# Performance work log

Measured on AMD Instinct MI355X. Metric: run time of the kernel, lower is better.

## Reference

```python
import jax, jax.numpy as jnp
import numpy as np

EPS = 1e-5

def setup_inputs() -> dict:
    key = jax.random.key(0)
    ks = jax.random.split(key, 8)
    N, C, ST, LT = 32, 2048, 16, 400
    ALPHA, K, BETA, CK = 4, 3, 4, 3
    Cb = C // BETA
    inp = {
        'st_feat': jax.random.normal(ks[0], (N, C, ST, 1, 1), dtype=jnp.float32),
        'lt_feat': jax.random.normal(ks[1], (N, C, LT, 1, 1), dtype=jnp.float32),
        # global branch G: Linear(ST->ST*alpha) -> BN1d -> ReLU -> Linear(->K) -> softmax
        'g_w1': jax.random.normal(ks[2], (ST * ALPHA, ST), dtype=jnp.float32) * 0.02,
        'g_bn_gamma': jnp.ones((ST * ALPHA,), jnp.float32),
        'g_bn_beta': jnp.zeros((ST * ALPHA,), jnp.float32),
        'g_bn_mean': jnp.zeros((ST * ALPHA,), jnp.float32),
        'g_bn_var': jnp.ones((ST * ALPHA,), jnp.float32),
        'g_w2': jax.random.normal(ks[3], (K, ST * ALPHA), dtype=jnp.float32) * 0.02,
        # local branch L: Conv1d(C->C/beta,k=3) -> BN1d -> ReLU -> Conv1d(C/beta->C,1) -> sigmoid
        'l_w1': jax.random.normal(ks[4], (Cb, C, CK), dtype=jnp.float32) * 0.02,
        'l_bn_gamma': jnp.ones((Cb,), jnp.float32),
        'l_bn_beta': jnp.zeros((Cb,), jnp.float32),
        'l_bn_mean': jnp.zeros((Cb,), jnp.float32),
        'l_bn_var': jnp.ones((Cb,), jnp.float32),
        'l_w2': jax.random.normal(ks[5], (C, Cb), dtype=jnp.float32) * 0.02,
    }
    return inp


def reference(st_feat, lt_feat, g_w1, g_bn_gamma, g_bn_beta, g_bn_mean, g_bn_var,
              g_w2, l_w1, l_bn_gamma, l_bn_beta, l_bn_mean, l_bn_var, l_w2):
    N, C, ST = st_feat.shape[:3]
    LT = lt_feat.shape[2]
    K = g_w2.shape[0]
    PAD = 1  # adaptive_convolution_padding; stride = 1
    # ---- global branch: per-(n,c) adaptive kernel (h=w=1 so avgpool is identity)
    st = st_feat.reshape(N * C, ST)                               # [NC, ST]
    h = st @ g_w1.T                                               # [NC, ST*alpha]
    h = (h - g_bn_mean) * jax.lax.rsqrt(g_bn_var + EPS) * g_bn_gamma + g_bn_beta
    h = jax.nn.relu(h)
    conv_kernel = jax.nn.softmax(h @ g_w2.T, axis=-1)             # [NC, K]
    # ---- local branch: channel-temporal sigmoid gate
    lt = lt_feat.reshape(N, C, LT)                                # [N, C, LT]
    x = jax.lax.conv_general_dilated(lt, l_w1, window_strides=(1,),
                                     padding=[(1, 1)],
                                     dimension_numbers=('NCH', 'OIH', 'NCH'))  # [N, C/beta, LT]
    x = (x - l_bn_mean[None, :, None]) * jax.lax.rsqrt(l_bn_var + EPS)[None, :, None] \
        * l_bn_gamma[None, :, None] + l_bn_beta[None, :, None]
    x = jax.nn.relu(x)
    gate = jax.nn.sigmoid(jnp.einsum('oc,nct->not', l_w2, x))     # [N, C, LT]
    new_lt = lt * gate
    # ---- temporal adaptive aggregation: per-(n,c) depthwise 1D conv, K taps
    kern = conv_kernel.reshape(N, C, K)
    xp = jnp.pad(new_lt, ((0, 0), (0, 0), (PAD, PAD)))            # [N, C, LT+2*PAD]
    out_len = LT + 2 * PAD - K + 1                                # == LT for K=3, PAD=1
    out = jnp.zeros((N, C, out_len), dtype=new_lt.dtype)
    for i in range(K):  # K is tiny (3)
        out = out + kern[:, :, i:i + 1] * xp[:, :, i:i + out_len]
    return out.reshape(N, C, out_len, 1, 1)
```

## Files before the change

kernel.cpp:

```cpp
#include <hip/hip_runtime.h>
#include <hip/hip_bf16.h>

#define N_   32
#define C_   2048
#define ST_  16
#define H_   64
#define K_   3
#define CB_  512
#define LT_  400
#define LTP_ 402
#define BK   32
#define TSTR 126

using bf16x8 = __attribute__((ext_vector_type(8))) __bf16;
using f32x4  = __attribute__((ext_vector_type(4))) float;
typedef unsigned short ushort_t;

__device__ __forceinline__ unsigned short f2bf(float f) {
    unsigned int u = __float_as_uint(f);
    u = (u + 0x7fffu + ((u >> 16) & 1u)) >> 16;
    return (unsigned short)u;
}
__device__ __forceinline__ float bf2f(unsigned short h) {
    return __uint_as_float(((unsigned int)h) << 16);
}
__device__ __forceinline__ void gload16(const ushort_t* g, ushort_t* l) {
    __builtin_amdgcn_global_load_lds(
        (const __attribute__((address_space(1))) unsigned int*)g,
        (__attribute__((address_space(3))) unsigned int*)l, 16, 0, 0);
}

__global__ __launch_bounds__(256) void k_global(
    const float* __restrict__ st, const float* __restrict__ g_w1,
    const float* __restrict__ gam, const float* __restrict__ bet,
    const float* __restrict__ mean, const float* __restrict__ var,
    const float* __restrict__ g_w2, float* __restrict__ kern) {
    __shared__ float w1[H_][ST_];
    __shared__ float sc[H_], bi[H_];
    __shared__ float w2[K_][H_];
    int tid = threadIdx.x;
    for (int i = tid; i < H_ * ST_; i += 256) w1[i / ST_][i % ST_] = g_w1[i];
    if (tid < H_) {
        float s = gam[tid] * rsqrtf(var[tid] + 1e-5f);
        sc[tid] = s;
        bi[tid] = bet[tid] - mean[tid] * s;
    }
    for (int i = tid; i < K_ * H_; i += 256) w2[i / H_][i % H_] = g_w2[i];
    __syncthreads();
    int row = blockIdx.x * 256 + tid;
    const float* p = st + (size_t)row * ST_;
    float s[ST_];
#pragma unroll
    for (int i = 0; i < ST_; ++i) s[i] = p[i];
    float lg0 = 0.f, lg1 = 0.f, lg2 = 0.f;
    for (int j = 0; j < H_; ++j) {
        float h = 0.f;
#pragma unroll
        for (int i = 0; i < ST_; ++i) h = fmaf(w1[j][i], s[i], h);
        h = fmaxf(fmaf(h, sc[j], bi[j]), 0.f);
        lg0 = fmaf(w2[0][j], h, lg0);
        lg1 = fmaf(w2[1][j], h, lg1);
        lg2 = fmaf(w2[2][j], h, lg2);
    }
    float m = fmaxf(lg0, fmaxf(lg1, lg2));
    float e0 = __expf(lg0 - m), e1 = __expf(lg1 - m), e2 = __expf(lg2 - m);
    float inv = 1.f / (e0 + e1 + e2);
    float4 o = make_float4(e0 * inv, e1 * inv, e2 * inv, 0.f);
    *(float4*)(kern + (size_t)row * 4) = o;
}

__global__ __launch_bounds__(256) void k_transpose(
    const float* __restrict__ lt, ushort_t* __restrict__ ltT) {
    __shared__ float tile[32][33];
    int tt0 = blockIdx.x * 32;
    int cc  = blockIdx.y * 32;
    int n   = blockIdx.z;
    const float* src = lt + ((size_t)n * C_ + cc) * LT_;
    int tx = threadIdx.x & 31, ty = threadIdx.x >> 5;
#pragma unroll
    for (int i = 0; i < 4; ++i) {
        int c = ty + i * 8;
        int t = tt0 + tx;
        tile[c][tx] = (t < LT_) ? src[(size_t)c * LT_ + t] : 0.f;
    }
    __syncthreads();
    int cx  = (threadIdx.x & 15) * 2;
    int tyw = threadIdx.x >> 4;
    unsigned int* dst = (unsigned int*)(ltT + (size_t)n * LTP_ * C_ + cc + cx);
#pragma unroll
    for (int i = 0; i < 2; ++i) {
        int tl = tyw + i * 16;
        int t = tt0 + tl;
        if (t < LT_) {
            unsigned int v = (unsigned int)f2bf(tile[cx][tl]) |
                             ((unsigned int)f2bf(tile[cx + 1][tl]) << 16);
            dst[(size_t)(t + 1) * (C_ / 2)] = v;
        }
    }
}

__global__ __launch_bounds__(256) void k_zero(ushort_t* __restrict__ ltT) {
    int i = blockIdx.x * 256 + threadIdx.x;
    int n = i >> 11, c = i & (C_ - 1);
    size_t base = (size_t)n * LTP_ * C_;
    ltT[base + c] = 0;
    ltT[base + (size_t)(LTP_ - 1) * C_ + c] = 0;
}

__global__ __launch_bounds__(256) void k_w1(
    const float* __restrict__ l_w1, ushort_t* __restrict__ w1b) {
    int i = blockIdx.x * 256 + threadIdx.x;
    float a = l_w1[(size_t)i * 3 + 0];
    float b = l_w1[(size_t)i * 3 + 1];
    float c = l_w1[(size_t)i * 3 + 2];
    w1b[0 * (size_t)CB_ * C_ + i] = f2bf(a);
    w1b[1 * (size_t)CB_ * C_ + i] = f2bf(b);
    w1b[2 * (size_t)CB_ * C_ + i] = f2bf(c);
}

__global__ __launch_bounds__(256) void k_w2(
    const float* __restrict__ l_w2, ushort_t* __restrict__ w2b) {
    int i = blockIdx.x * 256 + threadIdx.x;
    w2b[i] = f2bf(l_w2[i]);
}

__global__ __launch_bounds__(256, 2) void k_gemm1(
    const ushort_t* __restrict__ ltT, const ushort_t* __restrict__ w1b,
    const float* __restrict__ bn_g, const float* __restrict__ bn_b,
    const float* __restrict__ bn_m, const float* __restrict__ bn_v,
    ushort_t* __restrict__ Xws) {
    __shared__ __align__(16) ushort_t Asm[2 * 128 * BK];
    __shared__ __align__(16) ushort_t Bsm[2 * 384 * BK];
    const int tid = threadIdx.x;
    const int n   = blockIdx.z;
    const int tm  = blockIdx.x * TSTR;
    const int cb0 = blockIdx.y * 128;
    const int lane = tid & 63, lrow = lane & 15, quad = lane >> 4;
    const int wv = tid >> 6, wvM = wv & 1, wvN = wv >> 1;

    const int srow = lane >> 2;
    const int csrc = (((lane & 3) ^ ((lane >> 3) & 3)) << 3);
    const ushort_t* gA[2];
#pragma unroll
    for (int i = 0; i < 2; ++i) {
        int r = (2 * wv + i) * 16 + srow;
        int gr = tm + r; gr = gr < LTP_ - 1 ? gr : LTP_ - 1;
        gA[i] = ltT + ((size_t)n * LTP_ + gr) * C_ + csrc;
    }
    const ushort_t* gB[6];
#pragma unroll
    for (int j = 0; j < 6; ++j) {
        int r = (6 * wv + j) * 16 + srow;
        gB[j] = w1b + ((size_t)((r >> 7) * CB_ + cb0 + (r & 127))) * C_ + csrc;
    }
    const int sB = lrow * BK + ((quad ^ ((lrow >> 1) & 3)) << 3);
    int sA[3];
#pragma unroll
    for (int k = 0; k < 3; ++k)
        sA[k] = (lrow + k) * BK + ((quad ^ (((lrow + k) >> 1) & 3)) << 3);

    f32x4 acc[4][4];
#pragma unroll
    for (int i = 0; i < 4; ++i)
#pragma unroll
        for (int j = 0; j < 4; ++j) acc[i][j] = (f32x4){0.f, 0.f, 0.f, 0.f};

#define STAGE1(buf)                                                         \
    {                                                                       \
        ushort_t* ad = Asm + (buf) * (128 * BK) + (2 * wv) * (16 * BK);     \
        gload16(gA[0], ad);                                                 \
        gload16(gA[1], ad + 16 * BK);                                       \
        gA[0] += BK; gA[1] += BK;                                           \
        ushort_t* bd = Bsm + (buf) * (384 * BK) + (6 * wv) * (16 * BK);     \
        _Pragma("unroll")                                                   \
        for (int j = 0; j < 6; ++j) {                                       \
            gload16(gB[j], bd + j * (16 * BK));                             \
            gB[j] += BK;                                                    \
        }                                                                   \
    }

    STAGE1(0);
    for (int s = 0; s < C_ / BK; ++s) {
        __syncthreads();
        const int cur = s & 1;
        if (s + 1 < C_ / BK) STAGE1(cur ^ 1);
        const ushort_t* Ab = Asm + cur * (128 * BK) + wvM * (64 * BK);
        const ushort_t* Bb = Bsm + cur * (384 * BK) + wvN * (64 * BK) + sB;
        bf16x8 bfr[3][4];
#pragma unroll
        for (int k = 0; k < 3; ++k)
#pragma unroll
            for (int nf = 0; nf < 4; ++nf)
                bfr[k][nf] = *(const bf16x8*)(Bb + k * (128 * BK) + nf * (16 * BK));
#pragma unroll
        for (int mf = 0; mf < 4; ++mf) {
            bf16x8 af[3];
#pragma unroll
            for (int k = 0; k < 3; ++k)
                af[k] = *(const bf16x8*)(Ab + sA[k] + mf * (16 * BK));
#pragma unroll
            for (int nf = 0; nf < 4; ++nf)
#pragma unroll
                for (int k = 0; k < 3; ++k)
                    acc[mf][nf] = __builtin_amdgcn_mfma_f32_16x16x32_bf16(af[k], bfr[k][nf], acc[mf][nf], 0, 0, 0);
        }
    }
#undef STAGE1
    float sc[4], bo[4];
#pragma unroll
    for (int nf = 0; nf < 4; ++nf) {
        int cb = cb0 + wvN * 64 + nf * 16 + lrow;
        float s0 = bn_g[cb] * rsqrtf(bn_v[cb] + 1e-5f);
        sc[nf] = s0;
        bo[nf] = bn_b[cb] - bn_m[cb] * s0;
    }
#pragma unroll
    for (int mf = 0; mf < 4; ++mf) {
#pragma unroll
        for (int r = 0; r < 4; ++r) {
            int local = wvM * 64 + mf * 16 + quad * 4 + r;
            int t = tm + local;
            if (local < TSTR && t < LT_) {
#pragma unroll
                for (int nf = 0; nf < 4; ++nf) {
                    int cb = cb0 + wvN * 64 + nf * 16 + lrow;
                    float v = fmaxf(fmaf(acc[mf][nf][r], sc[nf], bo[nf]), 0.f);
                    Xws[((size_t)n * LT_ + t) * CB_ + cb] = f2bf(v);
                }
            }
        }
    }
}

__global__ __launch_bounds__(256, 3) void k_gemm2(
    const ushort_t* __restrict__ Xws, const ushort_t* __restrict__ w2b,
    ushort_t* __restrict__ gate) {
    __shared__ __align__(16) ushort_t Asm[2 * 128 * BK];
    __shared__ __align__(16) ushort_t Bsm[2 * 128 * BK];
    const int tid = threadIdx.x;
    const int n  = blockIdx.z;
    const int cm = blockIdx.x * 128;
    const int tt = blockIdx.y * 128;
    const int lane = tid & 63, lrow = lane & 15, quad = lane >> 4;
    const int wv = tid >> 6, wvM = wv & 1, wvN = wv >> 1;

    const int srow = lane >> 2;
    const int csrc = (((lane & 3) ^ ((lane >> 3) & 3)) << 3);
    const ushort_t* gA[2];
    const ushort_t* gB[2];
#pragma unroll
    for (int i = 0; i < 2; ++i) {
        int r = (2 * wv + i) * 16 + srow;
        gA[i] = w2b + (size_t)(cm + r) * CB_ + csrc;
        int tr = tt + r; tr = tr < LT_ - 1 ? tr : LT_ - 1;
        gB[i] = Xws + ((size_t)n * LT_ + tr) * CB_ + csrc;
    }
    const int sOff = lrow * BK + ((quad ^ ((lrow >> 1) & 3)) << 3);

    f32x4 acc[4][4];
#pragma unroll
    for (int i = 0; i < 4; ++i)
#pragma unroll
        for (int j = 0; j < 4; ++j) acc[i][j] = (f32x4){0.f, 0.f, 0.f, 0.f};

#define STAGE2(buf)                                                         \
    {                                                                       \
        ushort_t* ad = Asm + (buf) * (128 * BK) + (2 * wv) * (16 * BK);     \
        ushort_t* bd = Bsm + (buf) * (128 * BK) + (2 * wv) * (16 * BK);     \
        gload16(gA[0], ad);                                                 \
        gload16(gA[1], ad + 16 * BK);                                       \
        gload16(gB[0], bd);                                                 \
        gload16(gB[1], bd + 16 * BK);                                       \
        gA[0] += BK; gA[1] += BK; gB[0] += BK; gB[1] += BK;                 \
    }

    STAGE2(0);
    for (int s = 0; s < CB_ / BK; ++s) {
        __syncthreads();
        const int cur = s & 1;
        if (s + 1 < CB_ / BK) STAGE2(cur ^ 1);
        const ushort_t* Ab = Asm + cur * (128 * BK) + wvM * (64 * BK) + sOff;
        const ushort_t* Bb = Bsm + cur * (128 * BK) + wvN * (64 * BK) + sOff;
        bf16x8 af[4], bfm[4];
#pragma unroll
        for (int mf = 0; mf < 4; ++mf)
            af[mf] = *(const bf16x8*)(Ab + mf * (16 * BK));
#pragma unroll
        for (int nf = 0; nf < 4; ++nf)
            bfm[nf] = *(const bf16x8*)(Bb + nf * (16 * BK));
#pragma unroll
        for (int mf = 0; mf < 4; ++mf)
#pragma unroll
            for (int nf = 0; nf < 4; ++nf)
                acc[mf][nf] = __builtin_amdgcn_mfma_f32_16x16x32_bf16(af[mf], bfm[nf], acc[mf][nf], 0, 0, 0);
    }
#undef STAGE2
#pragma unroll
    for (int mf = 0; mf < 4; ++mf) {
#pragma unroll
        for (int r = 0; r < 4; ++r) {
            int c = cm + wvM * 64 + mf * 16 + quad * 4 + r;
#pragma unroll
            for (int nf = 0; nf < 4; ++nf) {
                int t = tt + wvN * 64 + nf * 16 + lrow;
                if (t < LT_) {
                    float g = 1.f / (1.f + __expf(-acc[mf][nf][r]));
                    gate[((size_t)n * C_ + c) * LT_ + t] = f2bf(g);
                }
            }
        }
    }
}

__global__ __launch_bounds__(256) void k_final(
    const float* __restrict__ lt, const ushort_t* __restrict__ gate,
    const float* __restrict__ kern, float* __restrict__ out) {
    long long idx = (long long)blockIdx.x * 256 + threadIdx.x;
    int t0 = (int)(idx % 100) * 4;
    long long nc = idx / 100;
    const float*   ltp = lt   + (size_t)nc * LT_;
    const ushort_t* gp = gate + (size_t)nc * LT_;
    float4 kv = *(const float4*)(kern + (size_t)nc * 4);
    float nl[6];
#pragma unroll
    for (int j = -1; j <= 4; ++j) {
        int t = t0 + j;
        nl[j + 1] = (t >= 0 && t < LT_) ? ltp[t] * bf2f(gp[t]) : 0.f;
    }
    float4 o;
    o.x = kv.x * nl[0] + kv.y * nl[1] + kv.z * nl[2];
    o.y = kv.x * nl[1] + kv.y * nl[2] + kv.z * nl[3];
    o.z = kv.x * nl[2] + kv.y * nl[3] + kv.z * nl[4];
    o.w = kv.x * nl[3] + kv.y * nl[4] + kv.z * nl[5];
    *(float4*)(out + (size_t)nc * LT_ + t0) = o;
}

extern "C" void kernel_launch(void* const* d_in, const int* in_sizes, int n_in,
                              void* d_out, int out_size, void* d_ws, size_t ws_size,
                              hipStream_t stream) {
    const float* st   = (const float*)d_in[0];
    const float* lt   = (const float*)d_in[1];
    const float* g_w1 = (const float*)d_in[2];
    const float* g_bg = (const float*)d_in[3];
    const float* g_bb = (const float*)d_in[4];
    const float* g_bm = (const float*)d_in[5];
    const float* g_bv = (const float*)d_in[6];
    const float* g_w2 = (const float*)d_in[7];
    const float* l_w1 = (const float*)d_in[8];
    const float* l_bg = (const float*)d_in[9];
    const float* l_bb = (const float*)d_in[10];
    const float* l_bm = (const float*)d_in[11];
    const float* l_bv = (const float*)d_in[12];
    const float* l_w2 = (const float*)d_in[13];
    float* out = (float*)d_out;

    char* ws = (char*)d_ws;
    float*    kern = (float*)(ws + 0);
    ushort_t* w1b  = (ushort_t*)(ws + 1048576);
    ushort_t* w2b  = (ushort_t*)(ws + 7340032);
    ushort_t* Xws  = (ushort_t*)(ws + 9437184);
    ushort_t* ltT  = (ushort_t*)(ws + 22544384);
    ushort_t* gate = ltT;

    k_global<<<dim3((N_ * C_) / 256), dim3(256), 0, stream>>>(
        st, g_w1, g_bg, g_bb, g_bm, g_bv, g_w2, kern);
    k_w1<<<dim3((CB_ * C_) / 256), dim3(256), 0, stream>>>(l_w1, w1b);
    k_w2<<<dim3((C_ * CB_) / 256), dim3(256), 0, stream>>>(l_w2, w2b);
    k_zero<<<dim3((N_ * C_) / 256), dim3(256), 0, stream>>>(ltT);
    k_transpose<<<dim3(13, C_ / 32, N_), dim3(256), 0, stream>>>(lt, ltT);
    k_gemm1<<<dim3(4, 4, N_), dim3(256), 0, stream>>>(
        ltT, w1b, l_bg, l_bb, l_bm, l_bv, Xws);
    k_gemm2<<<dim3(C_ / 128, 4, N_), dim3(256), 0, stream>>>(Xws, w2b, gate);
    k_final<<<dim3((N_ * C_ * (LT_ / 4)) / 256), dim3(256), 0, stream>>>(
        lt, gate, kern, out);
}
```

Measured before the change: 425.1 us.

## Triple-buffer GEMM pipelines, enlarge gemm1 tiles, flatten gemm2 over N*LT, widen final

Both GEMMs switch from double to triple-buffered LDS staging, using explicit vmcnt waits, raw barriers and setprio around the MFMA blocks so loads stay further in flight. gemm1 moves to 512-thread blocks covering 254 time rows each, so every batch needs two tiles instead of four and the large weight B tile is loaded half as often. gemm2 flattens batch and time into one dimension (12800 = 100*128), which removes the partial time tile and its wasted work. The final kernel processes 8 outputs per thread with vectorised loads. The extra LDS and 512-thread blocks may reduce occupancy.

```diff
diff --git a/kernel.cpp b/kernel.cpp
--- a/kernel.cpp
+++ b/kernel.cpp
@@ -10,7 +10,7 @@
 #define LT_  400
 #define LTP_ 402
 #define BK   32
-#define TSTR 126
+#define TV1  254
 
 using bf16x8 = __attribute__((ext_vector_type(8))) __bf16;
 using f32x4  = __attribute__((ext_vector_type(4))) float;
@@ -124,19 +124,21 @@
     w2b[i] = f2bf(l_w2[i]);
 }
 
-__global__ __launch_bounds__(256, 2) void k_gemm1(
+__global__ __launch_bounds__(512, 2) void k_gemm1(
     const ushort_t* __restrict__ ltT, const ushort_t* __restrict__ w1b,
     const float* __restrict__ bn_g, const float* __restrict__ bn_b,
     const float* __restrict__ bn_m, const float* __restrict__ bn_v,
     ushort_t* __restrict__ Xws) {
-    __shared__ __align__(16) ushort_t Asm[2 * 128 * BK];
-    __shared__ __align__(16) ushort_t Bsm[2 * 384 * BK];
+    __shared__ __align__(16) ushort_t Asm[3 * 256 * BK + 2 * BK];
+    __shared__ __align__(16) ushort_t Bsm[3 * 384 * BK];
     const int tid = threadIdx.x;
-    const int n   = blockIdx.z;
-    const int tm  = blockIdx.x * TSTR;
+    const int mseg = blockIdx.x;
+    const int n   = mseg >> 1;
+    const int tm  = (mseg & 1) * TV1;
     const int cb0 = blockIdx.y * 128;
     const int lane = tid & 63, lrow = lane & 15, quad = lane >> 4;
-    const int wv = tid >> 6, wvM = wv & 1, wvN = wv >> 1;
+    const int wv = tid >> 6;
+    const int wvM = wv >> 1, wvN = wv & 1;
 
     const int srow = lane >> 2;
     const int csrc = (((lane & 3) ^ ((lane >> 3) & 3)) << 3);
@@ -147,11 +149,11 @@
         int gr = tm + r; gr = gr < LTP_ - 1 ? gr : LTP_ - 1;
         gA[i] = ltT + ((size_t)n * LTP_ + gr) * C_ + csrc;
     }
-    const ushort_t* gB[6];
-#pragma unroll
-    for (int j = 0; j < 6; ++j) {
-        int r = (6 * wv + j) * 16 + srow;
-        gB[j] = w1b + ((size_t)((r >> 7) * CB_ + cb0 + (r & 127))) * C_ + csrc;
+    const ushort_t* gB[3];
+#pragma unroll
+    for (int j = 0; j < 3; ++j) {
+        int rB = (3 * wv + j) * 16 + srow;
+        gB[j] = w1b + ((size_t)((rB >> 7) * CB_ + cb0 + (rB & 127))) * C_ + csrc;
     }
     const int sB = lrow * BK + ((quad ^ ((lrow >> 1) & 3)) << 3);
     int sA[3];
@@ -167,24 +169,31 @@
 
 #define STAGE1(buf)                                                         \
     {                                                                       \
-        ushort_t* ad = Asm + (buf) * (128 * BK) + (2 * wv) * (16 * BK);     \
+        ushort_t* ad = Asm + (buf) * (256 * BK) + (2 * wv) * (16 * BK);     \
         gload16(gA[0], ad);                                                 \
         gload16(gA[1], ad + 16 * BK);                                       \
         gA[0] += BK; gA[1] += BK;                                           \
-        ushort_t* bd = Bsm + (buf) * (384 * BK) + (6 * wv) * (16 * BK);     \
-        _Pragma("unroll")                                                   \
-        for (int j = 0; j < 6; ++j) {                                       \
-            gload16(gB[j], bd + j * (16 * BK));                             \
-            gB[j] += BK;                                                    \
-        }                                                                   \
+        ushort_t* bd = Bsm + (buf) * (384 * BK) + (3 * wv) * (16 * BK);     \
+        gload16(gB[0], bd);                                                 \
+        gload16(gB[1], bd + 16 * BK);                                       \
+        gload16(gB[2], bd + 32 * BK);                                       \
+        gB[0] += BK; gB[1] += BK; gB[2] += BK;                              \
     }
 
     STAGE1(0);
+    STAGE1(1);
+    int cur = 0, pre = 2;
     for (int s = 0; s < C_ / BK; ++s) {
-        __syncthreads();
-        const int cur = s & 1;
-        if (s + 1 < C_ / BK) STAGE1(cur ^ 1);
-        const ushort_t* Ab = Asm + cur * (128 * BK) + wvM * (64 * BK);
+        if (s < C_ / BK - 1) asm volatile("s_waitcnt vmcnt(5)" ::: "memory");
+        else                 asm volatile("s_waitcnt vmcnt(0)" ::: "memory");
+        __builtin_amdgcn_sched_barrier(0);
+        __builtin_amdgcn_s_barrier();
+        __builtin_amdgcn_sched_barrier(0);
+        if (s < C_ / BK - 2) {
+            STAGE1(pre);
+            pre = (pre == 2) ? 0 : pre + 1;
+        }
+        const ushort_t* Ab = Asm + cur * (256 * BK) + wvM * (64 * BK);
         const ushort_t* Bb = Bsm + cur * (384 * BK) + wvN * (64 * BK) + sB;
         bf16x8 bfr[3][4];
 #pragma unroll
@@ -192,6 +201,7 @@
 #pragma unroll
             for (int nf = 0; nf < 4; ++nf)
                 bfr[k][nf] = *(const bf16x8*)(Bb + k * (128 * BK) + nf * (16 * BK));
+        __builtin_amdgcn_s_setprio(1);
 #pragma unroll
         for (int mf = 0; mf < 4; ++mf) {
             bf16x8 af[3];
@@ -204,6 +214,8 @@
                 for (int k = 0; k < 3; ++k)
                     acc[mf][nf] = __builtin_amdgcn_mfma_f32_16x16x32_bf16(af[k], bfr[k][nf], acc[mf][nf], 0, 0, 0);
         }
+        __builtin_amdgcn_s_setprio(0);
+        cur = (cur == 2) ? 0 : cur + 1;
     }
 #undef STAGE1
     float sc[4], bo[4];
@@ -220,7 +232,7 @@
         for (int r = 0; r < 4; ++r) {
             int local = wvM * 64 + mf * 16 + quad * 4 + r;
             int t = tm + local;
-            if (local < TSTR && t < LT_) {
+            if (local < TV1 && t < LT_) {
 #pragma unroll
                 for (int nf = 0; nf < 4; ++nf) {
                     int cb = cb0 + wvN * 64 + nf * 16 + lrow;
@@ -235,12 +247,11 @@
 __global__ __launch_bounds__(256, 3) void k_gemm2(
     const ushort_t* __restrict__ Xws, const ushort_t* __restrict__ w2b,
     ushort_t* __restrict__ gate) {
-    __shared__ __align__(16) ushort_t Asm[2 * 128 * BK];
-    __shared__ __align__(16) ushort_t Bsm[2 * 128 * BK];
+    __shared__ __align__(16) ushort_t Asm[3 * 128 * BK];
+    __shared__ __align__(16) ushort_t Bsm[3 * 128 * BK];
     const int tid = threadIdx.x;
-    const int n  = blockIdx.z;
-    const int cm = blockIdx.x * 128;
-    const int tt = blockIdx.y * 128;
+    const int cm  = blockIdx.x * 128;
+    const int fn0 = blockIdx.y * 128;
     const int lane = tid & 63, lrow = lane & 15, quad = lane >> 4;
     const int wv = tid >> 6, wvM = wv & 1, wvN = wv >> 1;
 
@@ -252,8 +263,7 @@
     for (int i = 0; i < 2; ++i) {
         int r = (2 * wv + i) * 16 + srow;
         gA[i] = w2b + (size_t)(cm + r) * CB_ + csrc;
-        int tr = tt + r; tr = tr < LT_ - 1 ? tr : LT_ - 1;
-        gB[i] = Xws + ((size_t)n * LT_ + tr) * CB_ + csrc;
+        gB[i] = Xws + (size_t)(fn0 + r) * CB_ + csrc;
     }
     const int sOff = lrow * BK + ((quad ^ ((lrow >> 1) & 3)) << 3);
 
@@ -275,10 +285,18 @@
     }
 
     STAGE2(0);
+    STAGE2(1);
+    int cur = 0, pre = 2;
     for (int s = 0; s < CB_ / BK; ++s) {
-        __syncthreads();
-        const int cur = s & 1;
-        if (s + 1 < CB_ / BK) STAGE2(cur ^ 1);
+        if (s < CB_ / BK - 1) asm volatile("s_waitcnt vmcnt(4)" ::: "memory");
+        else                  asm volatile("s_waitcnt vmcnt(0)" ::: "memory");
+        __builtin_amdgcn_sched_barrier(0);
+        __builtin_amdgcn_s_barrier();
+        __builtin_amdgcn_sched_barrier(0);
+        if (s < CB_ / BK - 2) {
+            STAGE2(pre);
+            pre = (pre == 2) ? 0 : pre + 1;
+        }
         const ushort_t* Ab = Asm + cur * (128 * BK) + wvM * (64 * BK) + sOff;
         const ushort_t* Bb = Bsm + cur * (128 * BK) + wvN * (64 * BK) + sOff;
         bf16x8 af[4], bfm[4];
@@ -288,11 +306,14 @@
 #pragma unroll
         for (int nf = 0; nf < 4; ++nf)
             bfm[nf] = *(const bf16x8*)(Bb + nf * (16 * BK));
+        __builtin_amdgcn_s_setprio(1);
 #pragma unroll
         for (int mf = 0; mf < 4; ++mf)
 #pragma unroll
             for (int nf = 0; nf < 4; ++nf)
                 acc[mf][nf] = __builtin_amdgcn_mfma_f32_16x16x32_bf16(af[mf], bfm[nf], acc[mf][nf], 0, 0, 0);
+        __builtin_amdgcn_s_setprio(0);
+        cur = (cur == 2) ? 0 : cur + 1;
     }
 #undef STAGE2
 #pragma unroll
@@ -302,11 +323,11 @@
             int c = cm + wvM * 64 + mf * 16 + quad * 4 + r;
 #pragma unroll
             for (int nf = 0; nf < 4; ++nf) {
-                int t = tt + wvN * 64 + nf * 16 + lrow;
-                if (t < LT_) {
-                    float g = 1.f / (1.f + __expf(-acc[mf][nf][r]));
-                    gate[((size_t)n * C_ + c) * LT_ + t] = f2bf(g);
-                }
+                unsigned fn = fn0 + wvN * 64 + nf * 16 + lrow;
+                unsigned nn = fn / LT_;
+                unsigned t  = fn - nn * LT_;
+                float g = 1.f / (1.f + __expf(-acc[mf][nf][r]));
+                gate[((size_t)nn * C_ + c) * LT_ + t] = f2bf(g);
             }
         }
     }
@@ -316,23 +337,41 @@
     const float* __restrict__ lt, const ushort_t* __restrict__ gate,
     const float* __restrict__ kern, float* __restrict__ out) {
     long long idx = (long long)blockIdx.x * 256 + threadIdx.x;
-    int t0 = (int)(idx % 100) * 4;
-    long long nc = idx / 100;
-    const float*   ltp = lt   + (size_t)nc * LT_;
-    const ushort_t* gp = gate + (size_t)nc * LT_;
+    int t0 = (int)(idx % 50) * 8;
+    long long nc = idx / 50;
+    const float*    ltp = lt   + (size_t)nc * LT_;
+    const ushort_t* gp  = gate + (size_t)nc * LT_;
     float4 kv = *(const float4*)(kern + (size_t)nc * 4);
-    float nl[6];
-#pragma unroll
-    for (int j = -1; j <= 4; ++j) {
-        int t = t0 + j;
-        nl[j + 1] = (t >= 0 && t < LT_) ? ltp[t] * bf2f(gp[t]) : 0.f;
-    }
-    float4 o;
-    o.x = kv.x * nl[0] + kv.y * nl[1] + kv.z * nl[2];
-    o.y = kv.x * nl[1] + kv.y * nl[2] + kv.z * nl[3];
-    o.z = kv.x * nl[2] + kv.y * nl[3] + kv.z * nl[4];
-    o.w = kv.x * nl[3] + kv.y * nl[4] + kv.z * nl[5];
-    *(float4*)(out + (size_t)nc * LT_ + t0) = o;
+    float4 va = *(const float4*)(ltp + t0);
+    float4 vb = *(const float4*)(ltp + t0 + 4);
+    float lm = (t0 > 0) ? ltp[t0 - 1] : 0.f;
+    float lp = (t0 + 8 < LT_) ? ltp[t0 + 8] : 0.f;
+    uint2 ga = *(const uint2*)(gp + t0);
+    uint2 gb = *(const uint2*)(gp + t0 + 4);
+    unsigned short gm = (t0 > 0) ? gp[t0 - 1] : (unsigned short)0;
+    unsigned short gq = (t0 + 8 < LT_) ? gp[t0 + 8] : (unsigned short)0;
+    float nl[10];
+    nl[0] = lm   * bf2f(gm);
+    nl[1] = va.x * bf2f((unsigned short)(ga.x & 0xffffu));
+    nl[2] = va.y * bf2f((unsigned short)(ga.x >> 16));
+    nl[3] = va.z * bf2f((unsigned short)(ga.y & 0xffffu));
+    nl[4] = va.w * bf2f((unsigned short)(ga.y >> 16));
+    nl[5] = vb.x * bf2f((unsigned short)(gb.x & 0xffffu));
+    nl[6] = vb.y * bf2f((unsigned short)(gb.x >> 16));
+    nl[7] = vb.z * bf2f((unsigned short)(gb.y & 0xffffu));
+    nl[8] = vb.w * bf2f((unsigned short)(gb.y >> 16));
+    nl[9] = lp   * bf2f(gq);
+    float4 o0, o1;
+    o0.x = kv.x * nl[0] + kv.y * nl[1] + kv.z * nl[2];
+    o0.y = kv.x * nl[1] + kv.y * nl[2] + kv.z * nl[3];
+    o0.z = kv.x * nl[2] + kv.y * nl[3] + kv.z * nl[4];
+    o0.w = kv.x * nl[3] + kv.y * nl[4] + kv.z * nl[5];
+    o1.x = kv.x * nl[4] + kv.y * nl[5] + kv.z * nl[6];
+    o1.y = kv.x * nl[5] + kv.y * nl[6] + kv.z * nl[7];
+    o1.z = kv.x * nl[6] + kv.y * nl[7] + kv.z * nl[8];
+    o1.w = kv.x * nl[7] + kv.y * nl[8] + kv.z * nl[9];
+    *(float4*)(out + (size_t)nc * LT_ + t0) = o0;
+    *(float4*)(out + (size_t)nc * LT_ + t0 + 4) = o1;
 }
 
 extern "C" void kernel_launch(void* const* d_in, const int* in_sizes, int n_in,
@@ -368,9 +407,9 @@
     k_w2<<<dim3((C_ * CB_) / 256), dim3(256), 0, stream>>>(l_w2, w2b);
     k_zero<<<dim3((N_ * C_) / 256), dim3(256), 0, stream>>>(ltT);
     k_transpose<<<dim3(13, C_ / 32, N_), dim3(256), 0, stream>>>(lt, ltT);
-    k_gemm1<<<dim3(4, 4, N_), dim3(256), 0, stream>>>(
+    k_gemm1<<<dim3(64, 4), dim3(512), 0, stream>>>(
         ltT, w1b, l_bg, l_bb, l_bm, l_bv, Xws);
-    k_gemm2<<<dim3(C_ / 128, 4, N_), dim3(256), 0, stream>>>(Xws, w2b, gate);
-    k_final<<<dim3((N_ * C_ * (LT_ / 4)) / 256), dim3(256), 0, stream>>>(
+    k_gemm2<<<dim3(C_ / 128, 100), dim3(256), 0, stream>>>(Xws, w2b, gate);
+    k_final<<<dim3((N_ * C_ * 50) / 256), dim3(256), 0, stream>>>(
         lt, gate, kern, out);
 }
```

Result: no change. 433.1 us (+1.9%).
